# Kernel tuning notes

Hardware: AMD Instinct MI355X
Metric: run time of the kernel (lower is better)

## Reference

```python
import jax, jax.numpy as jnp
import numpy as np

B, V = 8, 128  # batch, cubic volume side


def setup_inputs() -> dict:
    key = jax.random.key(0)
    k1, k2 = jax.random.split(key)
    input_volume1 = jax.random.normal(k1, (B, V, V, V), dtype=jnp.float32)
    input_volume2 = jax.random.normal(k2, (B, V, V, V), dtype=jnp.float32)
    return {"input_volume1": input_volume1, "input_volume2": input_volume2}


def reference(input_volume1, input_volume2):
    # Full circular 3D cross-correlation over all relative shifts:
    #   out[b, t] = sum_r v1[b, r] * v2[b, (r + t) mod V]  (t, r are 3D indices)
    # computed via the convolution theorem with real FFTs.
    axes = (1, 2, 3)
    f1 = jnp.fft.rfftn(input_volume1, axes=axes)          # [B, V, V, V//2+1] complex
    f2 = jnp.fft.rfftn(input_volume2, axes=axes)
    out = jnp.fft.irfftn(f1 * jnp.conj(f2), s=(V, V, V), axes=axes)
    return out.astype(jnp.float32)
```

## Files before the change

### kernel.cpp

```cpp
#include <hip/hip_runtime.h>
#include <math.h>


#define V    128
#define V2   16384
#define V3   2097152
#define NB   8
#define PFP  132
#define PH3  34
#define SLICE (V * PH3)

__device__ __forceinline__ int bitrev7(int x) {
  return (int)(__brev((unsigned)x) >> 25);
}
__device__ __forceinline__ int negrev(int j) {
  int k = bitrev7(j);
  return bitrev7((V - k) & (V - 1));
}

__device__ __forceinline__ float2 cmul(float2 a, float2 b) {
  return make_float2(a.x * b.x - a.y * b.y, a.x * b.y + a.y * b.x);
}
__device__ __forceinline__ float2 cmulc(float2 a, float2 b) {
  return make_float2(a.x * b.x + a.y * b.y, a.y * b.x - a.x * b.y);
}
__device__ __forceinline__ float2 csqr(float2 a) {
  return make_float2(a.x * a.x - a.y * a.y, 2.0f * a.x * a.y);
}
__device__ __forceinline__ float2 f2add(float2 a, float2 b) {
  return make_float2(a.x + b.x, a.y + b.y);
}
__device__ __forceinline__ float2 f2sub(float2 a, float2 b) {
  return make_float2(a.x - b.x, a.y - b.y);
}
__device__ __forceinline__ float2 NI(float2 z) { return make_float2(z.y, -z.x); }
__device__ __forceinline__ float2 PI(float2 z) { return make_float2(-z.y, z.x); }

template <int CTRL>
__device__ __forceinline__ float dppf(float v) {
  return __int_as_float(
      __builtin_amdgcn_update_dpp(0, __float_as_int(v), CTRL, 0xF, 0xF, true));
}
template <int CTRL>
__device__ __forceinline__ float2 dpp2(float2 v) {
  return make_float2(dppf<CTRL>(v.x), dppf<CTRL>(v.y));
}

struct WF16 {
  float2 T64[4], T32[2], T16a, T16b, T8w, ts4, ts2;
  float sg4, sg2, sg1;
  bool up4, up2;
  int e;

  __device__ void init(int lq) {
    e = lq ^ (((lq >> 2) & 1) * 3);
    const float k = -6.28318530717958647692f / 128.0f;
    float2 w1 = make_float2(cosf(k * (float)e), sinf(k * (float)e));
    const float C1 = 0.92387953251128675613f;
    const float S1 = 0.38268343236508977173f;
    const float R  = 0.70710678118654752440f;
    T64[0] = w1;
    T64[1] = cmul(w1, make_float2(C1, -S1));
    T64[2] = cmul(w1, make_float2(R, -R));
    T64[3] = cmul(w1, make_float2(S1, -C1));
    float2 w2 = csqr(w1);
    T32[0] = w2;
    T32[1] = cmul(w2, make_float2(R, -R));
    T16a = csqr(w2);
    T16b = NI(T16a);
    T8w = csqr(T16a);
    up4 = (e >> 2) & 1;
    up2 = (e >> 1) & 1;
    const bool up1 = e & 1;
    sg4 = up4 ? -1.0f : 1.0f;
    sg2 = up2 ? -1.0f : 1.0f;
    sg1 = up1 ? -1.0f : 1.0f;
    const int m4 = e & 3;
    float2 w8p = (m4 == 0) ? make_float2(1.0f, 0.0f)
               : (m4 == 1) ? make_float2(R, -R)
               : (m4 == 2) ? make_float2(0.0f, -1.0f)
                           : make_float2(-R, -R);
    ts4 = up4 ? w8p : make_float2(1.0f, 0.0f);
    ts2 = (up2 && (e & 1)) ? make_float2(0.0f, -1.0f) : make_float2(1.0f, 0.0f);
  }

  __device__ __forceinline__ void fwd(float2 c[16]) const {
#pragma unroll
    for (int j = 0; j < 8; ++j) {
      float2 u = c[j], v = c[j + 8];
      c[j] = f2add(u, v);
      float2 t = cmul(f2sub(u, v), T64[j & 3]);
      c[j + 8] = (j < 4) ? t : NI(t);
    }
#pragma unroll
    for (int g = 0; g < 2; ++g) {
#pragma unroll
      for (int j0 = 0; j0 < 4; ++j0) {
        const int j = g * 8 + j0;
        float2 u = c[j], v = c[j + 4];
        c[j] = f2add(u, v);
        float2 t = cmul(f2sub(u, v), T32[j0 & 1]);
        c[j + 4] = (j0 < 2) ? t : NI(t);
      }
    }
#pragma unroll
    for (int g = 0; g < 4; ++g) {
#pragma unroll
      for (int j0 = 0; j0 < 2; ++j0) {
        const int j = g * 4 + j0;
        float2 u = c[j], v = c[j + 2];
        c[j] = f2add(u, v);
        c[j + 2] = cmul(f2sub(u, v), j0 ? T16b : T16a);
      }
    }
#pragma unroll
    for (int j = 0; j < 16; j += 2) {
      float2 u = c[j], v = c[j + 1];
      c[j] = f2add(u, v);
      c[j + 1] = cmul(f2sub(u, v), T8w);
    }
#pragma unroll
    for (int j = 0; j < 16; ++j) {
      float2 p = dpp2<0x141>(c[j]);
      float2 t = make_float2(fmaf(c[j].x, sg4, p.x), fmaf(c[j].y, sg4, p.y));
      c[j] = cmul(t, ts4);
    }
#pragma unroll
    for (int j = 0; j < 16; ++j) {
      float2 p = dpp2<0x4E>(c[j]);
      float2 t = make_float2(fmaf(c[j].x, sg2, p.x), fmaf(c[j].y, sg2, p.y));
      c[j] = cmul(t, ts2);
    }
#pragma unroll
    for (int j = 0; j < 16; ++j) {
      float2 p = dpp2<0xB1>(c[j]);
      c[j] = make_float2(fmaf(c[j].x, sg1, p.x), fmaf(c[j].y, sg1, p.y));
    }
  }

  __device__ __forceinline__ void inv(float2 c[16]) const {
#pragma unroll
    for (int j = 0; j < 16; ++j) {
      float2 p = dpp2<0xB1>(c[j]);
      c[j] = make_float2(fmaf(c[j].x, sg1, p.x), fmaf(c[j].y, sg1, p.y));
    }
#pragma unroll
    for (int j = 0; j < 16; ++j) {
      float2 m = cmulc(c[j], ts2);
      float2 q = make_float2(up2 ? m.x : c[j].x, up2 ? m.y : c[j].y);
      float2 p = dpp2<0x4E>(q);
      c[j] = make_float2(fmaf(q.x, sg2, p.x), fmaf(q.y, sg2, p.y));
    }
#pragma unroll
    for (int j = 0; j < 16; ++j) {
      float2 m = cmulc(c[j], ts4);
      float2 q = make_float2(up4 ? m.x : c[j].x, up4 ? m.y : c[j].y);
      float2 p = dpp2<0x141>(q);
      c[j] = make_float2(fmaf(q.x, sg4, p.x), fmaf(q.y, sg4, p.y));
    }
#pragma unroll
    for (int j = 0; j < 16; j += 2) {
      float2 m = cmulc(c[j + 1], T8w);
      float2 u = c[j];
      c[j] = f2add(u, m);
      c[j + 1] = f2sub(u, m);
    }
#pragma unroll
    for (int g = 0; g < 4; ++g) {
#pragma unroll
      for (int j0 = 0; j0 < 2; ++j0) {
        const int j = g * 4 + j0;
        float2 m = cmulc(c[j + 2], j0 ? T16b : T16a);
        float2 u = c[j];
        c[j] = f2add(u, m);
        c[j + 2] = f2sub(u, m);
      }
    }
#pragma unroll
    for (int g = 0; g < 2; ++g) {
#pragma unroll
      for (int j0 = 0; j0 < 4; ++j0) {
        const int j = g * 8 + j0;
        float2 m0 = cmulc(c[j + 4], T32[j0 & 1]);
        float2 m = (j0 < 2) ? m0 : PI(m0);
        float2 u = c[j];
        c[j] = f2add(u, m);
        c[j + 4] = f2sub(u, m);
      }
    }
#pragma unroll
    for (int j = 0; j < 8; ++j) {
      float2 m0 = cmulc(c[j + 8], T64[j & 3]);
      float2 m = (j < 4) ? m0 : PI(m0);
      float2 u = c[j];
      c[j] = f2add(u, m);
      c[j + 8] = f2sub(u, m);
    }
  }
};

__global__ __launch_bounds__(1024) void k_fwd_xy(const float* __restrict__ v1,
                                                 const float* __restrict__ v2,
                                                 float2* __restrict__ Z) {
  __shared__ float2 s[V * PFP];
  const int tid = threadIdx.x, lane = tid & 63, wave = tid >> 6;
  const int o = lane >> 3, lq = lane & 7;
  const int b = blockIdx.x >> 6, zp = blockIdx.x & 63;
  const int z1 = zp * 2;
  WF16 F;
  F.init(lq);
  const int e = F.e;
  const int row = wave * 8 + o;
  float2 c[16];
  {
    const size_t g = (size_t)b * V3 + (size_t)z1 * V2 + (size_t)row * V;
#pragma unroll
    for (int j = 0; j < 16; ++j) {
      const int n = e + 8 * j;
      c[j] = make_float2(v1[g + n], v2[g + n]);
    }
    F.fwd(c);
#pragma unroll
    for (int j = 0; j < 16; ++j) s[row * PFP + e + 8 * j] = c[j];
  }
  __syncthreads();
  float pa[16], pb[16];
  {
    const size_t g = (size_t)b * V3 + (size_t)(z1 + 1) * V2 + (size_t)row * V;
#pragma unroll
    for (int j = 0; j < 16; ++j) {
      const int n = e + 8 * j;
      pa[j] = v1[g + n];
      pb[j] = v2[g + n];
    }
  }
  {
    float2 d[16];
#pragma unroll
    for (int j = 0; j < 16; ++j) d[j] = s[(e + 8 * j) * PFP + row];
    F.fwd(d);
    const size_t zb = ((size_t)(b * V + row) * V + z1) * V;
#pragma unroll
    for (int j = 0; j < 16; ++j) Z[zb + e + 8 * j] = d[j];
  }
  __syncthreads();
  {
#pragma unroll
    for (int j = 0; j < 16; ++j) c[j] = make_float2(pa[j], pb[j]);
    F.fwd(c);
#pragma unroll
    for (int j = 0; j < 16; ++j) s[row * PFP + e + 8 * j] = c[j];
  }
  __syncthreads();
  {
    float2 d[16];
#pragma unroll
    for (int j = 0; j < 16; ++j) d[j] = s[(e + 8 * j) * PFP + row];
    F.fwd(d);
    const size_t zb = ((size_t)(b * V + row) * V + (z1 + 1)) * V;
#pragma unroll
    for (int j = 0; j < 16; ++j) Z[zb + e + 8 * j] = d[j];
  }
}

__global__ __launch_bounds__(512, 4) void k_z_fused(float2* __restrict__ Z) {
  __shared__ float2 T[2 * SLICE];
  const int tid = threadIdx.x, lane = tid & 63, wave = tid >> 6;
  const int o = lane >> 3, lq = lane & 7;
  const int blk = blockIdx.x;
  const int b = blk >> 8, idx = blk & 255;
  int x0, x1, jb0, jb1;
  bool within = false;
  {
    const int h = idx >> 7, r2 = idx & 127;
    if (r2 < 126) {
      const int k = (r2 >> 1) + 1, cc = r2 & 1;
      const int xa = bitrev7(k), xb = bitrev7(V - k);
      if (h == 0) { x0 = xa; x1 = xb; jb0 = cc * 32; jb1 = cc * 32; }
      else { x0 = cc ? xb : xa; x1 = cc ? xa : xb; jb0 = 64; jb1 = 96; }
    } else {
      x0 = x1 = r2 - 126;
      if (h == 0) { jb0 = 0; jb1 = 32; within = true; }
      else { jb0 = 64; jb1 = 96; }
    }
  }
  WF16 F;
  F.init(lq);
  const int e = F.e;
  const size_t base0 = (size_t)(b * V + x0) * V2 + jb0;
  const size_t base1 = (size_t)(b * V + x1) * V2 + jb1;

  for (int p = tid; p < 2048; p += 512) {
    const int z = p >> 4, w = (p & 15) << 1;
    *(float4*)&T[z * PH3 + w] = *(const float4*)&Z[base0 + (size_t)z * V + w];
  }
  for (int p = tid; p < 2048; p += 512) {
    const int z = p >> 4, w = (p & 15) << 1;
    *(float4*)&T[SLICE + z * PH3 + w] =
        *(const float4*)&Z[base1 + (size_t)z * V + w];
  }
  __syncthreads();

  const int col = wave * 8 + o;
  const int tb = (col >> 5) * SLICE, yc = col & 31;
  float2 c[16];
#pragma unroll
  for (int j = 0; j < 16; ++j) c[j] = T[tb + (e + 8 * j) * PH3 + yc];
  F.fwd(c);
#pragma unroll
  for (int j = 0; j < 16; ++j) T[tb + (e + 8 * j) * PH3 + yc] = c[j];
  __syncthreads();

  if (!within) {
    for (int p = tid; p < 4096; p += 512) {
      const int z = p >> 5, t = p & 31;
      const int zm = negrev(z), tm = negrev(jb0 + t) & 31;
      const float2 a  = T[z * PH3 + t];
      const float2 bb = T[SLICE + zm * PH3 + tm];
      const float f1r = 0.5f * (a.x + bb.x), f1i = 0.5f * (a.y - bb.y);
      const float f2r = 0.5f * (a.y + bb.y), f2i = 0.5f * (bb.x - a.x);
      const float gr = f1r * f2r + f1i * f2i;
      const float gi = f1i * f2r - f1r * f2i;
      T[z * PH3 + t] = make_float2(gr, gi);
      T[SLICE + zm * PH3 + tm] = make_float2(gr, -gi);
    }
  } else {
    for (int p = tid; p < 8192; p += 512) {
      const int s2 = p >> 12, z = (p >> 5) & 127, t = p & 31;
      const int zm = negrev(z), tm = negrev(s2 * 32 + t) & 31;
      const int pl = z * 32 + t, pm = zm * 32 + tm;
      if (pm < pl) continue;
      const float2 a  = T[s2 * SLICE + z * PH3 + t];
      const float2 bb = T[s2 * SLICE + zm * PH3 + tm];
      const float f1r = 0.5f * (a.x + bb.x), f1i = 0.5f * (a.y - bb.y);
      const float f2r = 0.5f * (a.y + bb.y), f2i = 0.5f * (bb.x - a.x);
      const float gr = f1r * f2r + f1i * f2i;
      const float gi = f1i * f2r - f1r * f2i;
      T[s2 * SLICE + z * PH3 + t] = make_float2(gr, gi);
      if (pm != pl) T[s2 * SLICE + zm * PH3 + tm] = make_float2(gr, -gi);
    }
  }
  __syncthreads();

#pragma unroll
  for (int j = 0; j < 16; ++j) c[j] = T[tb + (e + 8 * j) * PH3 + yc];
  F.inv(c);
#pragma unroll
  for (int j = 0; j < 16; ++j) T[tb + (e + 8 * j) * PH3 + yc] = c[j];
  __syncthreads();

  for (int p = tid; p < 2048; p += 512) {
    const int z = p >> 4, w = (p & 15) << 1;
    *(float4*)&Z[base0 + (size_t)z * V + w] = *(const float4*)&T[z * PH3 + w];
  }
  for (int p = tid; p < 2048; p += 512) {
    const int z = p >> 4, w = (p & 15) << 1;
    *(float4*)&Z[base1 + (size_t)z * V + w] =
        *(const float4*)&T[SLICE + z * PH3 + w];
  }
}

__global__ __launch_bounds__(1024) void k_inv_xy(const float2* __restrict__ Z,
                                                 float* __restrict__ out) {
  __shared__ float2 s[V * PFP];
  const int tid = threadIdx.x, lane = tid & 63, wave = tid >> 6;
  const int o = lane >> 3, lq = lane & 7;
  const int b = blockIdx.x >> 6, zp = blockIdx.x & 63;
  const int z1 = zp * 2;
  WF16 F;
  F.init(lq);
  const int e = F.e;
  const int row = wave * 8 + o;
  const float sc = 1.0f / 2097152.0f;
  float2 c[16];
  const size_t zb0 = ((size_t)(b * V + row) * V + z1) * V;
  {
#pragma unroll
    for (int j = 0; j < 16; ++j) c[j] = Z[zb0 + e + 8 * j];
    F.inv(c);
#pragma unroll
    for (int j = 0; j < 16; ++j) s[(e + 8 * j) * PFP + row] = c[j];
  }
  __syncthreads();
  float2 pz[16];
  {
    const size_t zb1 = zb0 + V;
#pragma unroll
    for (int j = 0; j < 16; ++j) pz[j] = Z[zb1 + e + 8 * j];
  }
  {
    float2 d[16];
#pragma unroll
    for (int j = 0; j < 16; ++j) d[j] = s[row * PFP + e + 8 * j];
    F.inv(d);
    const size_t gg = (size_t)b * V3 + (size_t)z1 * V2 + (size_t)row * V;
#pragma unroll
    for (int j = 0; j < 16; ++j) out[gg + e + 8 * j] = d[j].x * sc;
  }
  __syncthreads();
  {
    F.inv(pz);
#pragma unroll
    for (int j = 0; j < 16; ++j) s[(e + 8 * j) * PFP + row] = pz[j];
  }
  __syncthreads();
  {
    float2 d[16];
#pragma unroll
    for (int j = 0; j < 16; ++j) d[j] = s[row * PFP + e + 8 * j];
    F.inv(d);
    const size_t gg = (size_t)b * V3 + (size_t)(z1 + 1) * V2 + (size_t)row * V;
#pragma unroll
    for (int j = 0; j < 16; ++j) out[gg + e + 8 * j] = d[j].x * sc;
  }
}

extern "C" void kernel_launch(void* const* d_in, const int* in_sizes, int n_in,
                              void* d_out, int out_size, void* d_ws, size_t ws_size,
                              hipStream_t stream) {
  const float* v1 = (const float*)d_in[0];
  const float* v2 = (const float*)d_in[1];
  float* out = (float*)d_out;
  float2* Z  = (float2*)d_ws;

  k_fwd_xy<<<NB * 64, 1024, 0, stream>>>(v1, v2, Z);
  k_z_fused<<<NB * 256, 512, 0, stream>>>(Z);
  k_inv_xy<<<NB * 64, 1024, 0, stream>>>(Z, out);
}
```

Measured before the change: 310.8 us.

## Restructure XY FFT kernels to one z-slice per 512-thread block with half-size LDS

The forward and inverse XY FFT kernels now process a single z-slice per block using 512 threads, each thread doing two row FFTs. The transpose through shared memory is split into two halves, so the LDS buffer shrinks to half the size. The aim is more resident blocks per CU (launch bounds 512,4) and twice as many blocks for better latency hiding. In exchange each thread holds two 16-point arrays, which raises register pressure, and each block needs an extra barrier round.

Result: slower. 346.0 us (+11.3%).

```diff
diff --git a/kernel.cpp b/kernel.cpp
--- a/kernel.cpp
+++ b/kernel.cpp
@@ -6,7 +6,8 @@
 #define V2   16384
 #define V3   2097152
 #define NB   8
-#define PFP  132
+#define P1   68
+#define P3   132
 #define PH3  34
 #define SLICE (V * PH3)
 
@@ -199,65 +200,57 @@
   }
 };
 
-__global__ __launch_bounds__(1024) void k_fwd_xy(const float* __restrict__ v1,
-                                                 const float* __restrict__ v2,
-                                                 float2* __restrict__ Z) {
-  __shared__ float2 s[V * PFP];
-  const int tid = threadIdx.x, lane = tid & 63, wave = tid >> 6;
-  const int o = lane >> 3, lq = lane & 7;
-  const int b = blockIdx.x >> 6, zp = blockIdx.x & 63;
-  const int z1 = zp * 2;
+__global__ __launch_bounds__(512, 4) void k_fwd_xy(const float* __restrict__ v1,
+                                                   const float* __restrict__ v2,
+                                                   float2* __restrict__ Z) {
+  __shared__ float2 s[V * P1];
+  const int tid = threadIdx.x;
+  const int g = tid >> 3, lq = tid & 7;
+  const int b = blockIdx.x >> 7, z1 = blockIdx.x & 127;
   WF16 F;
   F.init(lq);
   const int e = F.e;
-  const int row = wave * 8 + o;
-  float2 c[16];
-  {
-    const size_t g = (size_t)b * V3 + (size_t)z1 * V2 + (size_t)row * V;
-#pragma unroll
-    for (int j = 0; j < 16; ++j) {
-      const int n = e + 8 * j;
-      c[j] = make_float2(v1[g + n], v2[g + n]);
-    }
-    F.fwd(c);
-#pragma unroll
-    for (int j = 0; j < 16; ++j) s[row * PFP + e + 8 * j] = c[j];
-  }
-  __syncthreads();
-  float pa[16], pb[16];
-  {
-    const size_t g = (size_t)b * V3 + (size_t)(z1 + 1) * V2 + (size_t)row * V;
-#pragma unroll
-    for (int j = 0; j < 16; ++j) {
-      const int n = e + 8 * j;
-      pa[j] = v1[g + n];
-      pb[j] = v2[g + n];
-    }
-  }
+  const size_t pb = (size_t)b * V3 + (size_t)z1 * V2;
+  const size_t g0 = pb + (size_t)g * V, g1 = pb + (size_t)(g + 64) * V;
+  float2 c0[16], c1[16];
+#pragma unroll
+  for (int j = 0; j < 16; ++j) {
+    const int n = e + 8 * j;
+    c0[j] = make_float2(v1[g0 + n], v2[g0 + n]);
+  }
+#pragma unroll
+  for (int j = 0; j < 16; ++j) {
+    const int n = e + 8 * j;
+    c1[j] = make_float2(v1[g1 + n], v2[g1 + n]);
+  }
+  F.fwd(c0);
+  F.fwd(c1);
+#pragma unroll
+  for (int j = 0; j < 8; ++j) s[g * P1 + e + 8 * j] = c0[j];
+#pragma unroll
+  for (int j = 0; j < 8; ++j) s[(g + 64) * P1 + e + 8 * j] = c1[j];
+  __syncthreads();
   {
     float2 d[16];
 #pragma unroll
-    for (int j = 0; j < 16; ++j) d[j] = s[(e + 8 * j) * PFP + row];
+    for (int j = 0; j < 16; ++j) d[j] = s[(e + 8 * j) * P1 + g];
     F.fwd(d);
-    const size_t zb = ((size_t)(b * V + row) * V + z1) * V;
+    const size_t zb = ((size_t)(b * V + g) * V + z1) * V;
 #pragma unroll
     for (int j = 0; j < 16; ++j) Z[zb + e + 8 * j] = d[j];
   }
   __syncthreads();
-  {
-#pragma unroll
-    for (int j = 0; j < 16; ++j) c[j] = make_float2(pa[j], pb[j]);
-    F.fwd(c);
-#pragma unroll
-    for (int j = 0; j < 16; ++j) s[row * PFP + e + 8 * j] = c[j];
-  }
+#pragma unroll
+  for (int j = 8; j < 16; ++j) s[g * P1 + e + 8 * (j - 8)] = c0[j];
+#pragma unroll
+  for (int j = 8; j < 16; ++j) s[(g + 64) * P1 + e + 8 * (j - 8)] = c1[j];
   __syncthreads();
   {
     float2 d[16];
 #pragma unroll
-    for (int j = 0; j < 16; ++j) d[j] = s[(e + 8 * j) * PFP + row];
+    for (int j = 0; j < 16; ++j) d[j] = s[(e + 8 * j) * P1 + g];
     F.fwd(d);
-    const size_t zb = ((size_t)(b * V + row) * V + (z1 + 1)) * V;
+    const size_t zb = ((size_t)(b * V + 64 + g) * V + z1) * V;
 #pragma unroll
     for (int j = 0; j < 16; ++j) Z[zb + e + 8 * j] = d[j];
   }
@@ -360,56 +353,52 @@
   }
 }
 
-__global__ __launch_bounds__(1024) void k_inv_xy(const float2* __restrict__ Z,
-                                                 float* __restrict__ out) {
-  __shared__ float2 s[V * PFP];
-  const int tid = threadIdx.x, lane = tid & 63, wave = tid >> 6;
-  const int o = lane >> 3, lq = lane & 7;
-  const int b = blockIdx.x >> 6, zp = blockIdx.x & 63;
-  const int z1 = zp * 2;
+__global__ __launch_bounds__(512, 4) void k_inv_xy(const float2* __restrict__ Z,
+                                                   float* __restrict__ out) {
+  __shared__ float2 s[64 * P3];
+  const int tid = threadIdx.x;
+  const int g = tid >> 3, lq = tid & 7;
+  const int b = blockIdx.x >> 7, z1 = blockIdx.x & 127;
   WF16 F;
   F.init(lq);
   const int e = F.e;
-  const int row = wave * 8 + o;
+  const int x0 = g, x1 = g + 64;
+  const size_t zb0 = ((size_t)(b * V + x0) * V + z1) * V;
+  const size_t zb1 = ((size_t)(b * V + x1) * V + z1) * V;
+  float2 c0[16], c1[16];
+#pragma unroll
+  for (int j = 0; j < 16; ++j) c0[j] = Z[zb0 + e + 8 * j];
+#pragma unroll
+  for (int j = 0; j < 16; ++j) c1[j] = Z[zb1 + e + 8 * j];
+  F.inv(c0);
+  F.inv(c1);
+#pragma unroll
+  for (int j = 0; j < 8; ++j) s[(e + 8 * j) * P3 + x0] = c0[j];
+#pragma unroll
+  for (int j = 0; j < 8; ++j) s[(e + 8 * j) * P3 + x1] = c1[j];
+  __syncthreads();
   const float sc = 1.0f / 2097152.0f;
-  float2 c[16];
-  const size_t zb0 = ((size_t)(b * V + row) * V + z1) * V;
-  {
-#pragma unroll
-    for (int j = 0; j < 16; ++j) c[j] = Z[zb0 + e + 8 * j];
-    F.inv(c);
-#pragma unroll
-    for (int j = 0; j < 16; ++j) s[(e + 8 * j) * PFP + row] = c[j];
-  }
-  __syncthreads();
-  float2 pz[16];
-  {
-    const size_t zb1 = zb0 + V;
-#pragma unroll
-    for (int j = 0; j < 16; ++j) pz[j] = Z[zb1 + e + 8 * j];
-  }
   {
     float2 d[16];
 #pragma unroll
-    for (int j = 0; j < 16; ++j) d[j] = s[row * PFP + e + 8 * j];
+    for (int j = 0; j < 16; ++j) d[j] = s[g * P3 + e + 8 * j];
     F.inv(d);
-    const size_t gg = (size_t)b * V3 + (size_t)z1 * V2 + (size_t)row * V;
+    const size_t gg = (size_t)b * V3 + (size_t)z1 * V2 + (size_t)g * V;
 #pragma unroll
     for (int j = 0; j < 16; ++j) out[gg + e + 8 * j] = d[j].x * sc;
   }
   __syncthreads();
-  {
-    F.inv(pz);
-#pragma unroll
-    for (int j = 0; j < 16; ++j) s[(e + 8 * j) * PFP + row] = pz[j];
-  }
+#pragma unroll
+  for (int j = 8; j < 16; ++j) s[(e + 8 * (j - 8)) * P3 + x0] = c0[j];
+#pragma unroll
+  for (int j = 8; j < 16; ++j) s[(e + 8 * (j - 8)) * P3 + x1] = c1[j];
   __syncthreads();
   {
     float2 d[16];
 #pragma unroll
-    for (int j = 0; j < 16; ++j) d[j] = s[row * PFP + e + 8 * j];
+    for (int j = 0; j < 16; ++j) d[j] = s[g * P3 + e + 8 * j];
     F.inv(d);
-    const size_t gg = (size_t)b * V3 + (size_t)(z1 + 1) * V2 + (size_t)row * V;
+    const size_t gg = (size_t)b * V3 + (size_t)z1 * V2 + (size_t)(64 + g) * V;
 #pragma unroll
     for (int j = 0; j < 16; ++j) out[gg + e + 8 * j] = d[j].x * sc;
   }
@@ -423,7 +412,7 @@
   float* out = (float*)d_out;
   float2* Z  = (float2*)d_ws;
 
-  k_fwd_xy<<<NB * 64, 1024, 0, stream>>>(v1, v2, Z);
+  k_fwd_xy<<<NB * V, 512, 0, stream>>>(v1, v2, Z);
   k_z_fused<<<NB * 256, 512, 0, stream>>>(Z);
-  k_inv_xy<<<NB * 64, 1024, 0, stream>>>(Z, out);
-}
+  k_inv_xy<<<NB * V, 512, 0, stream>>>(Z, out);
+}
```

## Restructure XY FFT kernels: split forward by half-spectrum, one z-plane per block

Applied to the files above, without the earlier changes.

The forward XY kernel now splits each 128-point row FFT into even and odd halves by a first radix-2 decimation done at load time (sum and twiddled difference of rows g and g+64). Each of two blocks per plane then runs a 64-point column FFT and stages its output in shared memory so stores to Z are coalesced. The inverse XY kernel processes one z-plane per 1024-thread block instead of two and writes output through shared memory in coalesced float2 stores. Twiddle tables are replaced by a few base twiddles recomputed on the fly to cut register pressure. This adds more blocks and redundant input reads (each plane is read twice) in exchange for better occupancy and coalescing.

New measurement: 303.1 us. 2.5% less time.

```diff
diff --git a/kernel.cpp b/kernel.cpp
--- a/kernel.cpp
+++ b/kernel.cpp
@@ -6,7 +6,9 @@
 #define V2   16384
 #define V3   2097152
 #define NB   8
-#define PFP  132
+#define PR1  134
+#define PC1  66
+#define PR3  134
 #define PH3  34
 #define SLICE (V * PH3)
 
@@ -35,6 +37,10 @@
 }
 __device__ __forceinline__ float2 NI(float2 z) { return make_float2(z.y, -z.x); }
 __device__ __forceinline__ float2 PI(float2 z) { return make_float2(-z.y, z.x); }
+
+#define KC1 0.92387953251128675613f
+#define KS1 0.38268343236508977173f
+#define KR  0.70710678118654752440f
 
 template <int CTRL>
 __device__ __forceinline__ float dppf(float v) {
@@ -46,8 +52,8 @@
   return make_float2(dppf<CTRL>(v.x), dppf<CTRL>(v.y));
 }
 
-struct WF16 {
-  float2 T64[4], T32[2], T16a, T16b, T8w, ts4, ts2;
+struct WFT {
+  float2 w1, w2, w4, w8, ts4, ts2;
   float sg4, sg2, sg1;
   bool up4, up2;
   int e;
@@ -55,20 +61,10 @@
   __device__ void init(int lq) {
     e = lq ^ (((lq >> 2) & 1) * 3);
     const float k = -6.28318530717958647692f / 128.0f;
-    float2 w1 = make_float2(cosf(k * (float)e), sinf(k * (float)e));
-    const float C1 = 0.92387953251128675613f;
-    const float S1 = 0.38268343236508977173f;
-    const float R  = 0.70710678118654752440f;
-    T64[0] = w1;
-    T64[1] = cmul(w1, make_float2(C1, -S1));
-    T64[2] = cmul(w1, make_float2(R, -R));
-    T64[3] = cmul(w1, make_float2(S1, -C1));
-    float2 w2 = csqr(w1);
-    T32[0] = w2;
-    T32[1] = cmul(w2, make_float2(R, -R));
-    T16a = csqr(w2);
-    T16b = NI(T16a);
-    T8w = csqr(T16a);
+    w1 = make_float2(cosf(k * (float)e), sinf(k * (float)e));
+    w2 = csqr(w1);
+    w4 = csqr(w2);
+    w8 = csqr(w4);
     up4 = (e >> 2) & 1;
     up2 = (e >> 1) & 1;
     const bool up1 = e & 1;
@@ -77,21 +73,68 @@
     sg1 = up1 ? -1.0f : 1.0f;
     const int m4 = e & 3;
     float2 w8p = (m4 == 0) ? make_float2(1.0f, 0.0f)
-               : (m4 == 1) ? make_float2(R, -R)
+               : (m4 == 1) ? make_float2(KR, -KR)
                : (m4 == 2) ? make_float2(0.0f, -1.0f)
-                           : make_float2(-R, -R);
+                           : make_float2(-KR, -KR);
     ts4 = up4 ? w8p : make_float2(1.0f, 0.0f);
     ts2 = (up2 && (e & 1)) ? make_float2(0.0f, -1.0f) : make_float2(1.0f, 0.0f);
   }
 
-  __device__ __forceinline__ void fwd(float2 c[16]) const {
+  __device__ __forceinline__ void xf4(float2* c, int n) const {
+#pragma unroll
+    for (int j = 0; j < n; ++j) {
+      float2 p = dpp2<0x141>(c[j]);
+      float2 t = make_float2(fmaf(c[j].x, sg4, p.x), fmaf(c[j].y, sg4, p.y));
+      c[j] = cmul(t, ts4);
+    }
+#pragma unroll
+    for (int j = 0; j < n; ++j) {
+      float2 p = dpp2<0x4E>(c[j]);
+      float2 t = make_float2(fmaf(c[j].x, sg2, p.x), fmaf(c[j].y, sg2, p.y));
+      c[j] = cmul(t, ts2);
+    }
+#pragma unroll
+    for (int j = 0; j < n; ++j) {
+      float2 p = dpp2<0xB1>(c[j]);
+      c[j] = make_float2(fmaf(c[j].x, sg1, p.x), fmaf(c[j].y, sg1, p.y));
+    }
+  }
+  __device__ __forceinline__ void xi4(float2* c, int n) const {
+#pragma unroll
+    for (int j = 0; j < n; ++j) {
+      float2 p = dpp2<0xB1>(c[j]);
+      c[j] = make_float2(fmaf(c[j].x, sg1, p.x), fmaf(c[j].y, sg1, p.y));
+    }
+#pragma unroll
+    for (int j = 0; j < n; ++j) {
+      float2 m = cmulc(c[j], ts2);
+      float2 q = make_float2(up2 ? m.x : c[j].x, up2 ? m.y : c[j].y);
+      float2 p = dpp2<0x4E>(q);
+      c[j] = make_float2(fmaf(q.x, sg2, p.x), fmaf(q.y, sg2, p.y));
+    }
+#pragma unroll
+    for (int j = 0; j < n; ++j) {
+      float2 m = cmulc(c[j], ts4);
+      float2 q = make_float2(up4 ? m.x : c[j].x, up4 ? m.y : c[j].y);
+      float2 p = dpp2<0x141>(q);
+      c[j] = make_float2(fmaf(q.x, sg4, p.x), fmaf(q.y, sg4, p.y));
+    }
+  }
+
+  __device__ __forceinline__ void fwd128(float2 c[16]) const {
+    const float2 tA = cmul(w1, make_float2(KC1, -KS1));
+    const float2 tB = cmul(w1, make_float2(KR, -KR));
+    const float2 tC = cmul(w1, make_float2(KS1, -KC1));
 #pragma unroll
     for (int j = 0; j < 8; ++j) {
       float2 u = c[j], v = c[j + 8];
       c[j] = f2add(u, v);
-      float2 t = cmul(f2sub(u, v), T64[j & 3]);
+      const int q = j & 3;
+      float2 tw = (q == 0) ? w1 : (q == 1) ? tA : (q == 2) ? tB : tC;
+      float2 t = cmul(f2sub(u, v), tw);
       c[j + 8] = (j < 4) ? t : NI(t);
     }
+    const float2 t2 = cmul(w2, make_float2(KR, -KR));
 #pragma unroll
     for (int g = 0; g < 2; ++g) {
 #pragma unroll
@@ -99,10 +142,11 @@
         const int j = g * 8 + j0;
         float2 u = c[j], v = c[j + 4];
         c[j] = f2add(u, v);
-        float2 t = cmul(f2sub(u, v), T32[j0 & 1]);
+        float2 t = cmul(f2sub(u, v), (j0 & 1) ? t2 : w2);
         c[j + 4] = (j0 < 2) ? t : NI(t);
       }
     }
+    const float2 w4n = NI(w4);
 #pragma unroll
     for (int g = 0; g < 4; ++g) {
 #pragma unroll
@@ -110,57 +154,23 @@
         const int j = g * 4 + j0;
         float2 u = c[j], v = c[j + 2];
         c[j] = f2add(u, v);
-        c[j + 2] = cmul(f2sub(u, v), j0 ? T16b : T16a);
+        c[j + 2] = cmul(f2sub(u, v), j0 ? w4n : w4);
       }
     }
 #pragma unroll
     for (int j = 0; j < 16; j += 2) {
       float2 u = c[j], v = c[j + 1];
       c[j] = f2add(u, v);
-      c[j + 1] = cmul(f2sub(u, v), T8w);
-    }
-#pragma unroll
-    for (int j = 0; j < 16; ++j) {
-      float2 p = dpp2<0x141>(c[j]);
-      float2 t = make_float2(fmaf(c[j].x, sg4, p.x), fmaf(c[j].y, sg4, p.y));
-      c[j] = cmul(t, ts4);
-    }
-#pragma unroll
-    for (int j = 0; j < 16; ++j) {
-      float2 p = dpp2<0x4E>(c[j]);
-      float2 t = make_float2(fmaf(c[j].x, sg2, p.x), fmaf(c[j].y, sg2, p.y));
-      c[j] = cmul(t, ts2);
-    }
-#pragma unroll
-    for (int j = 0; j < 16; ++j) {
-      float2 p = dpp2<0xB1>(c[j]);
-      c[j] = make_float2(fmaf(c[j].x, sg1, p.x), fmaf(c[j].y, sg1, p.y));
-    }
-  }
-
-  __device__ __forceinline__ void inv(float2 c[16]) const {
-#pragma unroll
-    for (int j = 0; j < 16; ++j) {
-      float2 p = dpp2<0xB1>(c[j]);
-      c[j] = make_float2(fmaf(c[j].x, sg1, p.x), fmaf(c[j].y, sg1, p.y));
-    }
-#pragma unroll
-    for (int j = 0; j < 16; ++j) {
-      float2 m = cmulc(c[j], ts2);
-      float2 q = make_float2(up2 ? m.x : c[j].x, up2 ? m.y : c[j].y);
-      float2 p = dpp2<0x4E>(q);
-      c[j] = make_float2(fmaf(q.x, sg2, p.x), fmaf(q.y, sg2, p.y));
-    }
-#pragma unroll
-    for (int j = 0; j < 16; ++j) {
-      float2 m = cmulc(c[j], ts4);
-      float2 q = make_float2(up4 ? m.x : c[j].x, up4 ? m.y : c[j].y);
-      float2 p = dpp2<0x141>(q);
-      c[j] = make_float2(fmaf(q.x, sg4, p.x), fmaf(q.y, sg4, p.y));
-    }
+      c[j + 1] = cmul(f2sub(u, v), w8);
+    }
+    xf4(c, 16);
+  }
+
+  __device__ __forceinline__ void inv128(float2 c[16]) const {
+    xi4(c, 16);
 #pragma unroll
     for (int j = 0; j < 16; j += 2) {
-      float2 m = cmulc(c[j + 1], T8w);
+      float2 m = cmulc(c[j + 1], w8);
       float2 u = c[j];
       c[j] = f2add(u, m);
       c[j + 1] = f2sub(u, m);
@@ -170,100 +180,129 @@
 #pragma unroll
       for (int j0 = 0; j0 < 2; ++j0) {
         const int j = g * 4 + j0;
-        float2 m = cmulc(c[j + 2], j0 ? T16b : T16a);
+        float2 m0 = cmulc(c[j + 2], w4);
+        float2 m = j0 ? PI(m0) : m0;
         float2 u = c[j];
         c[j] = f2add(u, m);
         c[j + 2] = f2sub(u, m);
       }
     }
+    const float2 t2 = cmul(w2, make_float2(KR, -KR));
 #pragma unroll
     for (int g = 0; g < 2; ++g) {
 #pragma unroll
       for (int j0 = 0; j0 < 4; ++j0) {
         const int j = g * 8 + j0;
-        float2 m0 = cmulc(c[j + 4], T32[j0 & 1]);
+        float2 m0 = cmulc(c[j + 4], (j0 & 1) ? t2 : w2);
         float2 m = (j0 < 2) ? m0 : PI(m0);
         float2 u = c[j];
         c[j] = f2add(u, m);
         c[j + 4] = f2sub(u, m);
       }
     }
+    const float2 tA = cmul(w1, make_float2(KC1, -KS1));
+    const float2 tB = cmul(w1, make_float2(KR, -KR));
+    const float2 tC = cmul(w1, make_float2(KS1, -KC1));
 #pragma unroll
     for (int j = 0; j < 8; ++j) {
-      float2 m0 = cmulc(c[j + 8], T64[j & 3]);
+      const int q = j & 3;
+      float2 tw = (q == 0) ? w1 : (q == 1) ? tA : (q == 2) ? tB : tC;
+      float2 m0 = cmulc(c[j + 8], tw);
       float2 m = (j < 4) ? m0 : PI(m0);
       float2 u = c[j];
       c[j] = f2add(u, m);
       c[j + 8] = f2sub(u, m);
     }
   }
+
+  __device__ __forceinline__ void fwd64(float2 c[8]) const {
+    const float2 t2 = cmul(w2, make_float2(KR, -KR));
+#pragma unroll
+    for (int j = 0; j < 4; ++j) {
+      float2 u = c[j], v = c[j + 4];
+      c[j] = f2add(u, v);
+      float2 t = cmul(f2sub(u, v), (j & 1) ? t2 : w2);
+      c[j + 4] = (j < 2) ? t : NI(t);
+    }
+    const float2 w4n = NI(w4);
+#pragma unroll
+    for (int g = 0; g < 2; ++g) {
+#pragma unroll
+      for (int j0 = 0; j0 < 2; ++j0) {
+        const int j = g * 4 + j0;
+        float2 u = c[j], v = c[j + 2];
+        c[j] = f2add(u, v);
+        c[j + 2] = cmul(f2sub(u, v), j0 ? w4n : w4);
+      }
+    }
+#pragma unroll
+    for (int j = 0; j < 8; j += 2) {
+      float2 u = c[j], v = c[j + 1];
+      c[j] = f2add(u, v);
+      c[j + 1] = cmul(f2sub(u, v), w8);
+    }
+    xf4(c, 8);
+  }
 };
 
-__global__ __launch_bounds__(1024) void k_fwd_xy(const float* __restrict__ v1,
-                                                 const float* __restrict__ v2,
-                                                 float2* __restrict__ Z) {
-  __shared__ float2 s[V * PFP];
+__global__ __launch_bounds__(512) void k_fwd_xy(const float* __restrict__ v1,
+                                                const float* __restrict__ v2,
+                                                float2* __restrict__ Z) {
+  __shared__ float2 s[64 * PR1];
   const int tid = threadIdx.x, lane = tid & 63, wave = tid >> 6;
-  const int o = lane >> 3, lq = lane & 7;
-  const int b = blockIdx.x >> 6, zp = blockIdx.x & 63;
-  const int z1 = zp * 2;
-  WF16 F;
+  const int g = tid >> 3, lq = tid & 7;
+  const int bz = blockIdx.x >> 1, h = blockIdx.x & 1;
+  const int b = bz >> 7, z1 = bz & 127;
+  WFT F;
   F.init(lq);
   const int e = F.e;
-  const int row = wave * 8 + o;
+  const size_t pb = (size_t)b * V3 + (size_t)z1 * V2;
+  const float* __restrict__ a1 = v1 + pb + (size_t)g * V;
+  const float* __restrict__ a2 = v2 + pb + (size_t)g * V;
   float2 c[16];
-  {
-    const size_t g = (size_t)b * V3 + (size_t)z1 * V2 + (size_t)row * V;
+  if (h == 0) {
 #pragma unroll
     for (int j = 0; j < 16; ++j) {
       const int n = e + 8 * j;
-      c[j] = make_float2(v1[g + n], v2[g + n]);
-    }
-    F.fwd(c);
-#pragma unroll
-    for (int j = 0; j < 16; ++j) s[row * PFP + e + 8 * j] = c[j];
-  }
-  __syncthreads();
-  float pa[16], pb[16];
-  {
-    const size_t g = (size_t)b * V3 + (size_t)(z1 + 1) * V2 + (size_t)row * V;
+      c[j] = make_float2(a1[n] + a1[n + 64 * V], a2[n] + a2[n + 64 * V]);
+    }
+  } else {
+    const float kk = -6.28318530717958647692f / 128.0f;
+    const float2 Wg = make_float2(cosf(kk * (float)g), sinf(kk * (float)g));
 #pragma unroll
     for (int j = 0; j < 16; ++j) {
       const int n = e + 8 * j;
-      pa[j] = v1[g + n];
-      pb[j] = v2[g + n];
-    }
-  }
-  {
-    float2 d[16];
-#pragma unroll
-    for (int j = 0; j < 16; ++j) d[j] = s[(e + 8 * j) * PFP + row];
-    F.fwd(d);
-    const size_t zb = ((size_t)(b * V + row) * V + z1) * V;
-#pragma unroll
-    for (int j = 0; j < 16; ++j) Z[zb + e + 8 * j] = d[j];
-  }
-  __syncthreads();
-  {
-#pragma unroll
-    for (int j = 0; j < 16; ++j) c[j] = make_float2(pa[j], pb[j]);
-    F.fwd(c);
-#pragma unroll
-    for (int j = 0; j < 16; ++j) s[row * PFP + e + 8 * j] = c[j];
-  }
-  __syncthreads();
-  {
-    float2 d[16];
-#pragma unroll
-    for (int j = 0; j < 16; ++j) d[j] = s[(e + 8 * j) * PFP + row];
-    F.fwd(d);
-    const size_t zb = ((size_t)(b * V + row) * V + (z1 + 1)) * V;
-#pragma unroll
-    for (int j = 0; j < 16; ++j) Z[zb + e + 8 * j] = d[j];
-  }
-}
-
-__global__ __launch_bounds__(512, 4) void k_z_fused(float2* __restrict__ Z) {
+      float2 d = make_float2(a1[n] - a1[n + 64 * V], a2[n] - a2[n + 64 * V]);
+      c[j] = cmul(d, Wg);
+    }
+  }
+  F.fwd128(c);
+#pragma unroll
+  for (int j = 0; j < 16; ++j) s[g * PR1 + e + 8 * j] = c[j];
+  __syncthreads();
+  float2 ca[8], cb[8];
+#pragma unroll
+  for (int j = 0; j < 8; ++j) {
+    const int r = e + 8 * j;
+    ca[j] = s[r * PR1 + g];
+    cb[j] = s[r * PR1 + g + 64];
+  }
+  __syncthreads();
+  F.fwd64(ca);
+  F.fwd64(cb);
+#pragma unroll
+  for (int j = 0; j < 8; ++j) {
+    s[g * PC1 + e + 8 * j] = ca[j];
+    s[(g + 64) * PC1 + e + 8 * j] = cb[j];
+  }
+  __syncthreads();
+  for (int L = wave; L < 128; L += 8) {
+    const size_t zb = ((size_t)(b * V + L) * V + z1) * V + h * 64;
+    Z[zb + lane] = s[L * PC1 + lane];
+  }
+}
+
+__global__ __launch_bounds__(512) void k_z_fused(float2* __restrict__ Z) {
   __shared__ float2 T[2 * SLICE];
   const int tid = threadIdx.x, lane = tid & 63, wave = tid >> 6;
   const int o = lane >> 3, lq = lane & 7;
@@ -284,7 +323,7 @@
       else { jb0 = 64; jb1 = 96; }
     }
   }
-  WF16 F;
+  WFT F;
   F.init(lq);
   const int e = F.e;
   const size_t base0 = (size_t)(b * V + x0) * V2 + jb0;
@@ -306,7 +345,7 @@
   float2 c[16];
 #pragma unroll
   for (int j = 0; j < 16; ++j) c[j] = T[tb + (e + 8 * j) * PH3 + yc];
-  F.fwd(c);
+  F.fwd128(c);
 #pragma unroll
   for (int j = 0; j < 16; ++j) T[tb + (e + 8 * j) * PH3 + yc] = c[j];
   __syncthreads();
@@ -344,7 +383,7 @@
 
 #pragma unroll
   for (int j = 0; j < 16; ++j) c[j] = T[tb + (e + 8 * j) * PH3 + yc];
-  F.inv(c);
+  F.inv128(c);
 #pragma unroll
   for (int j = 0; j < 16; ++j) T[tb + (e + 8 * j) * PH3 + yc] = c[j];
   __syncthreads();
@@ -362,56 +401,38 @@
 
 __global__ __launch_bounds__(1024) void k_inv_xy(const float2* __restrict__ Z,
                                                  float* __restrict__ out) {
-  __shared__ float2 s[V * PFP];
+  __shared__ float2 s[V * PR3];
   const int tid = threadIdx.x, lane = tid & 63, wave = tid >> 6;
-  const int o = lane >> 3, lq = lane & 7;
-  const int b = blockIdx.x >> 6, zp = blockIdx.x & 63;
-  const int z1 = zp * 2;
-  WF16 F;
+  const int g = tid >> 3, lq = tid & 7;
+  const int b = blockIdx.x >> 7, z1 = blockIdx.x & 127;
+  WFT F;
   F.init(lq);
   const int e = F.e;
-  const int row = wave * 8 + o;
+  float2 c[16];
+  {
+    const size_t zb = ((size_t)(b * V + g) * V + z1) * V;
+#pragma unroll
+    for (int j = 0; j < 16; ++j) c[j] = Z[zb + e + 8 * j];
+    F.inv128(c);
+#pragma unroll
+    for (int j = 0; j < 16; ++j) s[(e + 8 * j) * PR3 + g] = c[j];
+  }
+  __syncthreads();
   const float sc = 1.0f / 2097152.0f;
-  float2 c[16];
-  const size_t zb0 = ((size_t)(b * V + row) * V + z1) * V;
   {
 #pragma unroll
-    for (int j = 0; j < 16; ++j) c[j] = Z[zb0 + e + 8 * j];
-    F.inv(c);
-#pragma unroll
-    for (int j = 0; j < 16; ++j) s[(e + 8 * j) * PFP + row] = c[j];
-  }
-  __syncthreads();
-  float2 pz[16];
-  {
-    const size_t zb1 = zb0 + V;
-#pragma unroll
-    for (int j = 0; j < 16; ++j) pz[j] = Z[zb1 + e + 8 * j];
-  }
-  {
-    float2 d[16];
-#pragma unroll
-    for (int j = 0; j < 16; ++j) d[j] = s[row * PFP + e + 8 * j];
-    F.inv(d);
-    const size_t gg = (size_t)b * V3 + (size_t)z1 * V2 + (size_t)row * V;
-#pragma unroll
-    for (int j = 0; j < 16; ++j) out[gg + e + 8 * j] = d[j].x * sc;
-  }
-  __syncthreads();
-  {
-    F.inv(pz);
-#pragma unroll
-    for (int j = 0; j < 16; ++j) s[(e + 8 * j) * PFP + row] = pz[j];
-  }
-  __syncthreads();
-  {
-    float2 d[16];
-#pragma unroll
-    for (int j = 0; j < 16; ++j) d[j] = s[row * PFP + e + 8 * j];
-    F.inv(d);
-    const size_t gg = (size_t)b * V3 + (size_t)(z1 + 1) * V2 + (size_t)row * V;
-#pragma unroll
-    for (int j = 0; j < 16; ++j) out[gg + e + 8 * j] = d[j].x * sc;
+    for (int j = 0; j < 16; ++j) c[j] = s[g * PR3 + e + 8 * j];
+    F.inv128(c);
+    float* fr = (float*)(s + g * PR3);
+#pragma unroll
+    for (int j = 0; j < 16; ++j)
+      fr[e + 8 * j] = c[j].x * sc;
+  }
+  __syncthreads();
+  for (int r = wave; r < 128; r += 16) {
+    const size_t gg = (size_t)b * V3 + (size_t)z1 * V2 + (size_t)r * V;
+    *(float2*)&out[gg + 2 * lane] =
+        *(const float2*)((const float*)(s + r * PR3) + 2 * lane);
   }
 }
 
@@ -423,7 +444,7 @@
   float* out = (float*)d_out;
   float2* Z  = (float2*)d_ws;
 
-  k_fwd_xy<<<NB * 64, 1024, 0, stream>>>(v1, v2, Z);
+  k_fwd_xy<<<NB * V * 2, 512, 0, stream>>>(v1, v2, Z);
   k_z_fused<<<NB * 256, 512, 0, stream>>>(Z);
-  k_inv_xy<<<NB * 64, 1024, 0, stream>>>(Z, out);
-}
+  k_inv_xy<<<NB * V, 1024, 0, stream>>>(Z, out);
+}
```
